# Optimization experiments

Measured on AMD Instinct MI355X. Metric: run time of the kernel, lower is better.

Reference implementation:

```python
import jax, jax.numpy as jnp
import numpy as np

B, S, E, H, T, VOCAB = 64, 512, 256, 512, 32, 32000

def setup_inputs():
    key = jax.random.key(0)
    ks = jax.random.split(key, 19)
    g = lambda i, shape: jax.random.normal(ks[i], shape, jnp.float32) * 0.05
    return {
        "sentence": jax.random.randint(ks[0], (S, B), 0, VOCAB),
        "emb_enc": g(1, (VOCAB, E)),
        "emb_dec": g(2, (VOCAB, E)),
        "W_ih": g(3, (4 * H, E)),
        "W_hh": g(4, (4 * H, H)),
        "b_ih": g(5, (4 * H,)),
        "b_hh": g(6, (4 * H,)),
        "dec_in0": g(7, (E,)),
        "Wx": g(8, (4 * H, E)),
        "bx": g(9, (4 * H,)),
        "Wh": g(10, (4 * H, H)),
        "bh": g(11, (4 * H,)),
        "W_out": g(12, (H, 2 * H)),
        "b_out": g(13, (H,)),
        "W_in": g(14, (H, H)),
        "b_in": g(15, (H,)),
        "W_ctx": g(16, (H, H)),
        "b_ctx": g(17, (H,)),
        "V": jax.random.uniform(ks[18], (H,), jnp.float32, -1.0, 1.0),
    }

def _lstm_cell(x, h, c, Wi, Whh, bi, bhh):
    # gate order i, f, g, o (matches torch LSTM and the decoder's chunk order)
    gates = x @ Wi.T + h @ Whh.T + bi + bhh
    i, f, g, o = jnp.split(gates, 4, axis=-1)
    c_t = jax.nn.sigmoid(f) * c + jax.nn.sigmoid(i) * jnp.tanh(g)
    h_t = jax.nn.sigmoid(o) * jnp.tanh(c_t)
    return h_t, c_t

def _pointer_net(sentence, emb_enc, emb_dec, W_ih, W_hh, b_ih, b_hh, dec_in0,
                 Wx, bx, Wh, bh, W_out, b_out, W_in, b_in, W_ctx, b_ctx, V):
    s_len, b = sentence.shape
    h_dim = W_hh.shape[1]
    embs = emb_enc[sentence]                          # [S, B, E]
    h0 = jnp.zeros((b, h_dim), embs.dtype)
    c0 = jnp.zeros((b, h_dim), embs.dtype)

    def enc_step(carry, x_t):
        h, c = _lstm_cell(x_t, carry[0], carry[1], W_ih, W_hh, b_ih, b_hh)
        return (h, c), h

    (h_n, c_n), enc_out = jax.lax.scan(enc_step, (h0, c0), embs)   # enc_out [S, B, H]
    context = enc_out.transpose(1, 0, 2)              # [B, S, H]
    # conv1d(kernel=1) projection of the context; constant across decode steps
    ctx = jnp.einsum('bsh,gh->bgs', context, W_ctx) + b_ctx[None, :, None]  # [B, H, S]

    dec_embs = emb_dec[sentence].transpose(1, 0, 2)   # [B, S, E]
    pos = jnp.arange(s_len)

    def dec_step(carry, _):
        dec_in, h, c, mask = carry
        h_t, c_t = _lstm_cell(dec_in, h, c, Wx, Wh, bx, bh)
        inp = h_t @ W_in.T + b_in                      # [B, H]
        att = jnp.einsum('h,bhs->bs', V, jnp.tanh(inp[:, :, None] + ctx))
        att = jnp.where(mask == 0, -jnp.inf, att)
        alpha = jax.nn.softmax(att, axis=1)            # [B, S]
        hidden_state = jnp.einsum('bhs,bs->bh', ctx, alpha)
        h_new = jnp.tanh(jnp.concatenate([hidden_state, h_t], axis=1) @ W_out.T + b_out)
        idx = jnp.argmax(alpha * mask, axis=1)         # greedy pointer, first max on ties
        one_hot = (pos[None, :] == idx[:, None]).astype(alpha.dtype)
        mask_new = mask * (1.0 - one_hot)
        next_in = jnp.take_along_axis(dec_embs, idx[:, None, None], axis=1)[:, 0, :]
        return (next_in, h_new, c_t, mask_new), (alpha, idx)

    mask0 = jnp.ones((b, s_len), embs.dtype)
    dec_in0_b = jnp.broadcast_to(dec_in0, (b, dec_in0.shape[0]))
    _, (alphas, ptrs) = jax.lax.scan(dec_step, (dec_in0_b, h_n, c_n, mask0), None, length=T)
    return alphas.transpose(1, 0, 2), ptrs.T          # [B, T, S], [B, T]

def reference(sentence, emb_enc, emb_dec, W_ih, W_hh, b_ih, b_hh, dec_in0,
              Wx, bx, Wh, bh, W_out, b_out, W_in, b_in, W_ctx, b_ctx, V):
    return _pointer_net(sentence, emb_enc, emb_dec, W_ih, W_hh, b_ih, b_hh, dec_in0,
                        Wx, bx, Wh, bh, W_out, b_out, W_in, b_in, W_ctx, b_ctx, V)
```

## Files before the change

### kernel.cpp

```cpp
#include <hip/hip_runtime.h>
#include <hip/hip_bf16.h>


typedef unsigned short u16;
typedef unsigned long long u64;
typedef __bf16 bf16_t;
typedef bf16_t bf16x8 __attribute__((ext_vector_type(8)));
typedef float f32x4 __attribute__((ext_vector_type(4)));

#define MFMA16(a, b, c) __builtin_amdgcn_mfma_f32_16x16x32_bf16(a, b, c, 0, 0, 0)
#define AGENT __HIP_MEMORY_SCOPE_AGENT

#define FLG_OFF   64u
#define GENE_OFF  128u
#define LDE_OFF   192u
#define FLE_OFF   1216u
#define GEND_OFF  11456u
#define LDD_OFF   11520u
#define FLD_OFF   12544u
#define BAR_END   28928u
#define HE_OFF    32768u
#define CW_OFF    294912u
#define HD_OFF    425984u
#define AO_OFF    557056u
#define INP_OFF   819200u
#define ATT_OFF   950272u
#define MSK_OFF   1081344u
#define PAC_OFF   1212416u
#define PML_OFF   1736704u
#define DIN_OFF   1740800u
#define CTX_OFF   2097152u
#define CTXL_OFF  (CTX_OFF + 33554432u)
#define NEED_T0   (CTX_OFF + 67108864u)
#define NEED_T1   (CTX_OFF + 50331648u)
#define NEED_T2   (CTX_OFF + 33554432u)

__device__ __forceinline__ float bf2f(u16 b) {
  union { unsigned u; float f; } c; c.u = ((unsigned)b) << 16; return c.f;
}
__device__ __forceinline__ u16 f2bf(float x) {
  union { float f; unsigned u; } c; c.f = x;
  unsigned r = c.u + 0x7FFFu + ((c.u >> 16) & 1u);
  return (u16)(r >> 16);
}
__device__ __forceinline__ float sigf(float x) { return 1.0f / (1.0f + expf(-x)); }
__device__ __forceinline__ float sel4(float a0, float a1, float a2, float a3, int j) {
  float r = (j == 1) ? a1 : a0;
  r = (j == 2) ? a2 : r;
  r = (j == 3) ? a3 : r;
  return r;
}
__device__ __forceinline__ float wget(const void* p, long i, int f32m) {
  return f32m ? ((const float*)p)[i] : bf2f(((const u16*)p)[i]);
}
__device__ __forceinline__ void ld8(const void* p, long i, int f32m, float (&o)[8]) {
  if (f32m) {
    const float4* q = (const float4*)((const float*)p + i);
    float4 a = q[0], b = q[1];
    o[0] = a.x; o[1] = a.y; o[2] = a.z; o[3] = a.w;
    o[4] = b.x; o[5] = b.y; o[6] = b.z; o[7] = b.w;
  } else {
    uint4 u = *(const uint4*)((const u16*)p + i);
    unsigned ww[4] = {u.x, u.y, u.z, u.w};
#pragma unroll
    for (int k = 0; k < 4; ++k) {
      o[2 * k] = bf2f((u16)(ww[k] & 0xFFFFu));
      o[2 * k + 1] = bf2f((u16)(ww[k] >> 16));
    }
  }
}
__device__ __forceinline__ float ald(const float* p) {
  return __hip_atomic_load(p, __ATOMIC_RELAXED, AGENT);
}
__device__ __forceinline__ void ast(float* p, float v) {
  __hip_atomic_store(p, v, __ATOMIC_RELAXED, AGENT);
}
__device__ __forceinline__ int aldi(const int* p) {
  return __hip_atomic_load(p, __ATOMIC_RELAXED, AGENT);
}
__device__ __forceinline__ void ld8T(const float* T, int kb, int bA, float (&o)[8]) {
  const float* p = T + kb * 64 + bA;
#pragma unroll
  for (int j = 0; j < 8; ++j) o[j] = ald(p + j * 64);
}

__device__ __forceinline__ void split3(float x, u16& h, u16& l, u16& l2) {
  union { float f; unsigned u; } c; c.f = x;
  h = (u16)(c.u >> 16);
  float r = x - bf2f(h);
  union { float f; unsigned u; } e; e.f = r;
  l = (u16)(e.u >> 16);
  float r2 = r - bf2f(l);
  union { float f; unsigned u; } g; g.f = r2;
  l2 = (u16)(g.u >> 16);
}
__device__ __forceinline__ void split8v(const float (&a)[8], bf16x8& H, bf16x8& L,
                                        bf16x8& L2) {
  union { unsigned u[4]; bf16x8 v; } hh, ll, mm;
#pragma unroll
  for (int k = 0; k < 4; ++k) {
    union { float f; unsigned u; } x0, x1;
    x0.f = a[2 * k]; x1.f = a[2 * k + 1];
    unsigned t0 = x0.u & 0xFFFF0000u, t1 = x1.u & 0xFFFF0000u;
    union { unsigned u; float f; } b0, b1; b0.u = t0; b1.u = t1;
    float r0 = x0.f - b0.f, r1 = x1.f - b1.f;
    union { float f; unsigned u; } e0, e1; e0.f = r0; e1.f = r1;
    unsigned s0 = e0.u & 0xFFFF0000u, s1 = e1.u & 0xFFFF0000u;
    union { unsigned u; float f; } c0, c1; c0.u = s0; c1.u = s1;
    float q0 = r0 - c0.f, q1 = r1 - c1.f;
    union { float f; unsigned u; } g0, g1; g0.f = q0; g1.f = q1;
    hh.u[k] = t1 | (x0.u >> 16);
    ll.u[k] = s1 | (e0.u >> 16);
    mm.u[k] = (g1.u & 0xFFFF0000u) | (g0.u >> 16);
  }
  H = hh.v; L = ll.v; L2 = mm.v;
}
// ... 4 lines not shown
  acc = MFMA16(al, bh, acc);
  acc = MFMA16(ah, bl, acc);
  acc = MFMA16(al, bl, acc);
  acc = MFMA16(ah, bl2, acc);
  acc = MFMA16(al2, bh, acc);
  return acc;
}
__device__ __forceinline__ f32x4 groupMMv(const float (&a8)[8], const u16* B3c, int bo,
                                          f32x4 acc) {
  bf16x8 H, L, L2;
  split8v(a8, H, L, L2);
  return mfma6(H, L, L2, *(const bf16x8*)(B3c + bo), *(const bf16x8*)(B3c + 4224 + bo),
               *(const bf16x8*)(B3c + 8448 + bo), acc);
}
__device__ __forceinline__ void stage16(u16* B3, const void* W, int f32m,
                                        long src, int n, int k16) {
  float t0[8], t1[8];
  ld8(W, src, f32m, t0);
  ld8(W, src + 8, f32m, t1);
#pragma unroll
  for (int j = 0; j < 8; ++j) {
    u16 h, l, l2; split3(t0[j], h, l, l2);
    int o = n * 264 + k16 + j;
    B3[o] = h; B3[4224 + o] = l; B3[8448 + o] = l2;
  }
#pragma unroll
  for (int j = 0; j < 8; ++j) {
    u16 h, l, l2; split3(t1[j], h, l, l2);
    int o = n * 264 + k16 + 8 + j;
    B3[o] = h; B3[4224 + o] = l; B3[8448 + o] = l2;
  }
}

__device__ __forceinline__ void ctx_store(char* ws, int tier, int oi, float x) {
  if (tier == 0) { ((float*)(ws + CTX_OFF))[oi] = x; return; }
  if (tier >= 3) return;
  u16 hi = f2bf(x);
  ((u16*)(ws + CTX_OFF))[oi] = hi;
  if (tier == 1) {
    unsigned e = hi & 0x7F80u; if (e == 0) e = 0x0080u;
    float us = bf2f((u16)e) * 0.00390625f;
    float r = (x - bf2f(hi)) / us;
    int q = (int)__float2int_rn(r * 254.0f);
    q = max(-127, min(127, q));
    ((signed char*)(ws + CTXL_OFF))[oi] = (signed char)q;
  }
}
__device__ __forceinline__ void ctx_load8(const char* ws, int tier, int oi, float (&cx)[8]) {
  if (tier == 0) {
    const float4* p = (const float4*)((const float*)(ws + CTX_OFF) + oi);
    float4 a = p[0], b = p[1];
    cx[0] = a.x; cx[1] = a.y; cx[2] = a.z; cx[3] = a.w;
    cx[4] = b.x; cx[5] = b.y; cx[6] = b.z; cx[7] = b.w;
    return;
  }
  if (tier >= 3) {
#pragma unroll
    for (int j = 0; j < 8; ++j) cx[j] = 0.0f;
    return;
  }
  uint4 hu = *(const uint4*)((const u16*)(ws + CTX_OFF) + oi);
  unsigned hw[4] = {hu.x, hu.y, hu.z, hu.w};
  u16 h[8];
#pragma unroll
  for (int k = 0; k < 4; ++k) { h[2*k] = (u16)(hw[k] & 0xFFFFu); h[2*k+1] = (u16)(hw[k] >> 16); }
#pragma unroll
  for (int j = 0; j < 8; ++j) cx[j] = bf2f(h[j]);
  if (tier == 1) {
    const signed char* lp = (const signed char*)(ws + CTXL_OFF) + oi;
#pragma unroll
    for (int j = 0; j < 8; ++j) {
      unsigned e = h[j] & 0x7F80u; if (e == 0) e = 0x0080u;
      float us = bf2f((u16)e) * 0.00390625f;
      cx[j] += (float)lp[j] * us * (1.0f / 254.0f);
    }
  }
}

__device__ __forceinline__ void fbar_arrive(char* ws, unsigned flOff, int wg, int gen) {
  __builtin_amdgcn_s_waitcnt(0);
  __syncthreads();
  if (threadIdx.x == 0)
    __hip_atomic_store((int*)(ws + flOff) + wg * 16, gen, __ATOMIC_RELAXED, AGENT);
}
__device__ __forceinline__ void fbar_wait(char* ws, unsigned flOff, int nwg, int gen) {
  const int tid = threadIdx.x;
  if (tid < 64) {
    const int* fl = (const int*)(ws + flOff);
    for (int i = tid; i < nwg; i += 64) {
      const int* f = fl + i * 16;
      while (aldi(f) < gen) __builtin_amdgcn_s_sleep(1);
    }
  }
  __syncthreads();
}

__global__ void prep_detect(const void* embE, char* ws) {
  __shared__ int cnt;
  if (threadIdx.x == 0) cnt = 0;
  __syncthreads();
  const u16* p = (const u16*)embE;
  int c = 0;
  for (int i = threadIdx.x; i < 4096; i += 256) {
    float v = bf2f(p[i]);
    if (!(fabsf(v) < 4.0f)) c++;
  }
  atomicAdd(&cnt, c);
  __syncthreads();
  if (threadIdx.x == 0) *(int*)(ws + FLG_OFF) = (cnt > 200) ? 1 : 0;
}

__global__ void prep_init(const void* din0, char* ws) {
  const int f32m = *(const int*)(ws + FLG_OFF);
  int i0 = blockIdx.x * 256 + threadIdx.x;
  int stride = gridDim.x * 256;
  int* bars = (int*)ws;
  for (int i = i0; i < (int)((BAR_END - GENE_OFF) / 4); i += stride)
    bars[(GENE_OFF / 4) + i] = 0;
  float* h0 = (float*)(ws + HE_OFF);
  float* mask = (float*)(ws + MSK_OFF);
  float* dinT = (float*)(ws + DIN_OFF);
  for (int i = i0; i < 32768; i += stride) { h0[i] = 0.0f; mask[i] = 1.0f; }
  for (int i = i0; i < 16384; i += stride) dinT[i] = wget(din0, i >> 6, f32m);
}

__global__ __launch_bounds__(256, 1) void enc_pers(
    const int* __restrict__ sent, const void* __restrict__ embE,
    const void* __restrict__ Wih, const void* __restrict__ Whh,
    const void* __restrict__ bih, const void* __restrict__ bhh,
    const void* __restrict__ Wctx, const void* __restrict__ bctx,
    char* __restrict__ ws, int tier) {
  __shared__ __align__(16) u16 B3[38016];
  const int tid = threadIdx.x, w = blockIdx.x;
  const int f32m = *(const int*)(ws + FLG_OFF);
  const int lane = tid & 63, v = tid >> 6, ln15 = lane & 15, q = lane >> 4;
  const int bA = v * 16 + ln15;
  const int sn = tid >> 4, sk = (tid & 15) * 16;
  float* heT = (float*)(ws + HE_OFF);
  float* cwp = (float*)(ws + CW_OFF);

  const int g = ln15 & 3;
  const int unit = w * 4 + (ln15 >> 2);
  float creg[4];
#pragma unroll
  for (int r = 0; r < 4; ++r) creg[r] = 0.0f;
  float bias = 0.0f;

  if (w < 128) {
    long grC = (long)(g * 512 + unit);
    bias = wget(bih, grC, f32m) + wget(bhh, grC, f32m);
    const long grS = (long)((sn & 3) * 512 + w * 4 + (sn >> 2));
    stage16(B3, Wih, f32m, grS * 256 + sk, sn, sk);
    stage16(B3 + 12672, Whh, f32m, grS * 512 + sk, sn, sk);
    stage16(B3 + 25344, Whh, f32m, grS * 512 + 256 + sk, sn, sk);
  } else {
    const long grS = (long)((w - 128) * 16 + sn);
    stage16(B3, Wctx, f32m, grS * 512 + sk, sn, sk);
    stage16(B3 + 12672, Wctx, f32m, grS * 512 + 256 + sk, sn, sk);
  }
  __syncthreads();

#pragma unroll 1
  for (int t = 0; t < 512; ++t) {
    const int slot = t & 1;
    const float* hsT = heT + slot * 32768;
    if (w < 128) {
      const int tok = sent[t * 64 + bA];
      f32x4 acc = {0.f, 0.f, 0.f, 0.f};
      {
        float aE[4][8];
#pragma unroll
        for (int pf = 0; pf < 3; ++pf)
          ld8(embE, (long)tok * 256 + pf * 32 + q * 8, f32m, aE[pf]);
#pragma unroll
        for (int ks = 0; ks < 8; ++ks) {
          if (ks + 3 < 8) ld8(embE, (long)tok * 256 + (ks + 3) * 32 + q * 8, f32m,
                              aE[(ks + 3) & 3]);
          acc = groupMMv(aE[ks & 3], B3, ln15 * 264 + ks * 32 + q * 8, acc);
        }
      }
      if (t) fbar_wait(ws, FLE_OFF, 160, t);
      {
        float aH[4][8];
#pragma unroll
        for (int pf = 0; pf < 3; ++pf) ld8T(hsT, pf * 32 + q * 8, bA, aH[pf]);
#pragma unroll
        for (int kk = 0; kk < 16; ++kk) {
          if (kk + 3 < 16) ld8T(hsT, (kk + 3) * 32 + q * 8, bA, aH[(kk + 3) & 3]);
          acc = groupMMv(aH[kk & 3], B3 + (1 + (kk >> 3)) * 12672,
                         ln15 * 264 + (kk & 7) * 32 + q * 8, acc);
        }
      }
      float* hdTs = heT + (slot ^ 1) * 32768;
#pragma unroll
      for (int r = 0; r < 4; ++r) {
        int br = v * 16 + q * 4 + r;
        float val = acc[r] + bias;
        float x1 = __shfl_xor(val, 1);
        float x2 = __shfl_xor(val, 2);
        float x3 = __shfl_xor(val, 3);
        float gi = sel4(val, x1, x2, x3, g);
        float gf = sel4(val, x1, x2, x3, g ^ 1);
        float gg = sel4(val, x1, x2, x3, g ^ 2);
        float go = sel4(val, x1, x2, x3, g ^ 3);
        float cn = sigf(gf) * creg[r] + sigf(gi) * tanhf(gg);
        float hv = sigf(go) * tanhf(cn);
        creg[r] = cn;
        if (g == 0) ast(hdTs + unit * 64 + br, hv);
      }
    } else {
      if (t) {
        fbar_wait(ws, FLE_OFF, 160, t);
        float aH[4][8];
#pragma unroll
        for (int pf = 0; pf < 3; ++pf) ld8T(hsT, pf * 32 + q * 8, bA, aH[pf]);
        f32x4 acc = {0.f, 0.f, 0.f, 0.f};
#pragma unroll
        for (int kk = 0; kk < 16; ++kk) {
          if (kk + 3 < 16) ld8T(hsT, (kk + 3) * 32 + q * 8, bA, aH[(kk + 3) & 3]);
          acc = groupMMv(aH[kk & 3], B3 + (kk >> 3) * 12672,
                         ln15 * 264 + (kk & 7) * 32 + q * 8, acc);
        }
        const int d = (w - 128) * 16 + ln15;
        float bb = wget(bctx, d, f32m);
#pragma unroll
        for (int r = 0; r < 4; ++r) {
          int br = v * 16 + q * 4 + r;
          ctx_store(ws, tier, (br * 512 + (t - 1)) * 512 + d, acc[r] + bb);
        }
      }
    }
    fbar_arrive(ws, FLE_OFF, w, t + 1);
  }
  if (w >= 128) {
    fbar_wait(ws, FLE_OFF, 160, 512);
    const float* hsT = heT;
    float aH[4][8];
#pragma unroll
    for (int pf = 0; pf < 3; ++pf) ld8T(hsT, pf * 32 + q * 8, bA, aH[pf]);
    f32x4 acc = {0.f, 0.f, 0.f, 0.f};
#pragma unroll
    for (int kk = 0; kk < 16; ++kk) {
      if (kk + 3 < 16) ld8T(hsT, (kk + 3) * 32 + q * 8, bA, aH[(kk + 3) & 3]);
      acc = groupMMv(aH[kk & 3], B3 + (kk >> 3) * 12672,
                     ln15 * 264 + (kk & 7) * 32 + q * 8, acc);
    }
    const int d = (w - 128) * 16 + ln15;
    float bb = wget(bctx, d, f32m);
#pragma unroll
    for (int r = 0; r < 4; ++r) {
      int br = v * 16 + q * 4 + r;
      ctx_store(ws, tier, (br * 512 + 511) * 512 + d, acc[r] + bb);
    }
  } else if (g == 0) {
#pragma unroll
    for (int r = 0; r < 4; ++r) cwp[(v * 16 + q * 4 + r) * 512 + unit] = creg[r];
  }
}

__global__ __launch_bounds__(256, 1) void dec_pers(
    const int* __restrict__ sent, const void* __restrict__ embD,
    const void* __restrict__ Wx, const void* __restrict__ bx,
    const void* __restrict__ Wh, const void* __restrict__ bh,
    const void* __restrict__ Wout, const void* __restrict__ bout,
    const void* __restrict__ Win, const void* __restrict__ bin,
    const void* __restrict__ V, char* __restrict__ ws,
    float* __restrict__ out, int tier) {
  __shared__ __align__(16) u16 B3[50688];
  __shared__ float accL[512];
  __shared__ float mlL[8];
  __shared__ float redA[256];
  __shared__ int redI[256];

  const int tid = threadIdx.x, wg = blockIdx.x;
  const int f32m = *(const int*)(ws + FLG_OFF);
  const int lane = tid & 63, v = tid >> 6, ln15 = lane & 15, q = lane >> 4;
  const int bA = v * 16 + ln15;
  const int sn = tid >> 4, sk = (tid & 15) * 16;
  float* hdT = (float*)(ws + HD_OFF);
  float* aoT = (float*)(ws + AO_OFF);
  float* inp = (float*)(ws + INP_OFF);
  float* att = (float*)(ws + ATT_OFF);
  float* mask = (float*)(ws + MSK_OFF);
  float* pac = (float*)(ws + PAC_OFF);
  float* pml = (float*)(ws + PML_OFF);
  float* dinT = (float*)(ws + DIN_OFF);
  const float* hnT = (const float*)(ws + HE_OFF);
  int bgen = 0;

  const int g = ln15 & 3;
  const int unit = (wg < 128) ? (wg * 4 + (ln15 >> 2)) : 0;
  float creg[4];
  float bias = 0.0f;
  if (wg < 128) {
    const float* cwp = (const float*)(ws + CW_OFF);
#pragma unroll
    for (int r = 0; r < 4; ++r) creg[r] = cwp[(v * 16 + q * 4 + r) * 512 + unit];
    bias = wget(bx, (long)(g * 512 + unit), f32m) + wget(bh, (long)(g * 512 + unit), f32m);
  }
  float vj[8];
#pragma unroll
  for (int j = 0; j < 8; ++j) vj[j] = wget(V, lane * 8 + j, f32m);

  if (wg < 128) {
    const long grS = (long)((sn & 3) * 512 + wg * 4 + (sn >> 2));
    stage16(B3, Wx, f32m, grS * 256 + sk, sn, sk);
    stage16(B3 + 12672, Wh, f32m, grS * 512 + sk, sn, sk);
    stage16(B3 + 25344, Wh, f32m, grS * 512 + 256 + sk, sn, sk);
  } else if (wg < 160) {
    const long grS = (long)((wg - 128) * 16 + sn);
    stage16(B3, Win, f32m, grS * 512 + sk, sn, sk);
    stage16(B3 + 12672, Win, f32m, grS * 512 + 256 + sk, sn, sk);
  } else if (wg < 192) {
    const long grS = (long)((wg - 160) * 16 + sn);
#pragma unroll
    for (int cc = 0; cc < 4; ++cc)
      stage16(B3 + cc * 12672, Wout, f32m, grS * 1024 + cc * 256 + sk, sn, sk);
  }
  __syncthreads();

  f32x4 acc1 = {0.f, 0.f, 0.f, 0.f};
  if (wg < 128) {
    float aD[4][8];
#pragma unroll
    for (int pf = 0; pf < 3; ++pf) ld8T(dinT, pf * 32 + q * 8, bA, aD[pf]);
#pragma unroll
    for (int ks = 0; ks < 8; ++ks) {
      if (ks + 3 < 8) ld8T(dinT, (ks + 3) * 32 + q * 8, bA, aD[(ks + 3) & 3]);
      acc1 = groupMMv(aD[ks & 3], B3, ln15 * 264 + ks * 32 + q * 8, acc1);
    }
  }

#pragma unroll 1
  for (int t = 0; t < 32; ++t) {
    if (wg < 128) {
      const float* hsT = (t == 0) ? hnT : (const float*)hdT;
      float aH[4][8];
#pragma unroll
      for (int pf = 0; pf < 3; ++pf) ld8T(hsT, pf * 32 + q * 8, bA, aH[pf]);
#pragma unroll
      for (int kk = 0; kk < 16; ++kk) {
        if (kk + 3 < 16) ld8T(hsT, (kk + 3) * 32 + q * 8, bA, aH[(kk + 3) & 3]);
        acc1 = groupMMv(aH[kk & 3], B3 + (1 + (kk >> 3)) * 12672,
                        ln15 * 264 + (kk & 7) * 32 + q * 8, acc1);
      }
#pragma unroll
      for (int r = 0; r < 4; ++r) {
        int br = v * 16 + q * 4 + r;
        float val = acc1[r] + bias;
        float x1 = __shfl_xor(val, 1);
        float x2 = __shfl_xor(val, 2);
        float x3 = __shfl_xor(val, 3);
        float gi = sel4(val, x1, x2, x3, g);
        float gf = sel4(val, x1, x2, x3, g ^ 1);
        float gg = sel4(val, x1, x2, x3, g ^ 2);
        float go = sel4(val, x1, x2, x3, g ^ 3);
        float cn = sigf(gf) * creg[r] + sigf(gi) * tanhf(gg);
        float hv = sigf(go) * tanhf(cn);
        creg[r] = cn;
        if (g == 0) ast(aoT + (512 + unit) * 64 + br, hv);
      }
    }
    ++bgen;
    fbar_arrive(ws, FLD_OFF, wg, bgen);
    fbar_wait(ws, FLD_OFF, 256, bgen);
    if (wg >= 128 && wg < 160) {
      float aH[4][8];
#pragma unroll
      for (int pf = 0; pf < 3; ++pf) ld8T(aoT, 512 + pf * 32 + q * 8, bA, aH[pf]);
      f32x4 acc = {0.f, 0.f, 0.f, 0.f};
#pragma unroll
      for (int kk = 0; kk < 16; ++kk) {
        if (kk + 3 < 16) ld8T(aoT, 512 + (kk + 3) * 32 + q * 8, bA, aH[(kk + 3) & 3]);
        acc = groupMMv(aH[kk & 3], B3 + (kk >> 3) * 12672,
                       ln15 * 264 + (kk & 7) * 32 + q * 8, acc);
      }
      const int d = (wg - 128) * 16 + ln15;
      float bb = wget(bin, d, f32m);
#pragma unroll
      for (int r = 0; r < 4; ++r)
        ast(inp + (v * 16 + q * 4 + r) * 512 + d, acc[r] + bb);
    }
    ++bgen;
    fbar_arrive(ws, FLD_OFF, wg, bgen);
    const int b = wg & 63, qq = wg >> 6;
    const int s0 = qq * 128 + v * 32;
    float mkB[4];
    float cxB[4][8];
#pragma unroll
    for (int pf = 0; pf < 3; ++pf) {
      mkB[pf] = ald(mask + b * 512 + s0 + pf);
      ctx_load8(ws, tier, (b * 512 + s0 + pf) * 512 + lane * 8, cxB[pf]);
    }
    fbar_wait(ws, FLD_OFF, 256, bgen);
    {
      float ij[8];
#pragma unroll
      for (int j = 0; j < 8; ++j) ij[j] = ald(inp + b * 512 + lane * 8 + j);
      for (int i = tid; i < 512; i += 256) accL[i] = 0.0f;
      __syncthreads();
      float m = -1e30f, l = 0.0f;
      float oacc[8];
#pragma unroll
      for (int j = 0; j < 8; ++j) oacc[j] = 0.0f;
#pragma unroll 1
      for (int i0 = 0; i0 < 32; ++i0) {
        const int s = s0 + i0;
        if (i0 + 3 < 32) {
          mkB[(i0 + 3) & 3] = ald(mask + b * 512 + s + 3);
          ctx_load8(ws, tier, (b * 512 + s + 3) * 512 + lane * 8, cxB[(i0 + 3) & 3]);
        }
        float mkC = mkB[i0 & 3];
        const float (&cxC)[8] = cxB[i0 & 3];
        if (mkC == 0.0f) {
          if (lane == 0) ast(att + b * 512 + s, -1e30f);
        } else {
          float p = 0.0f;
#pragma unroll
          for (int j = 0; j < 8; ++j) p += vj[j] * tanhf(ij[j] + cxC[j]);
#pragma unroll
          for (int off = 1; off < 64; off <<= 1) p += __shfl_xor(p, off);
          if (lane == 0) ast(att + b * 512 + s, p);
          if (p <= m) {
            float e = expf(p - m);
            l += e;
#pragma unroll
            for (int j = 0; j < 8; ++j) oacc[j] += e * cxC[j];
          } else {
            float sc = expf(m - p);
            l = l * sc + 1.0f;
#pragma unroll
            for (int j = 0; j < 8; ++j) oacc[j] = oacc[j] * sc + cxC[j];
            m = p;
          }
        }
      }
      if (lane == 0) { mlL[v * 2] = m; mlL[v * 2 + 1] = l; }
      __syncthreads();
      float M = fmaxf(fmaxf(mlL[0], mlL[2]), fmaxf(mlL[4], mlL[6]));
      float Lq = 0.0f;
#pragma unroll
      for (int vv = 0; vv < 4; ++vv) Lq += mlL[vv * 2 + 1] * expf(mlL[vv * 2] - M);
      float scv = expf(m - M);
      for (int vv = 0; vv < 4; ++vv) {
        if (v == vv) {
#pragma unroll
          for (int j = 0; j < 8; ++j) accL[lane * 8 + j] += oacc[j] * scv;
        }
        __syncthreads();
      }
      for (int i = tid; i < 512; i += 256) ast(pac + (b * 4 + qq) * 512 + i, accL[i]);
      if (tid == 0) {
        ast(pml + (b * 4 + qq) * 2, M);
        ast(pml + (b * 4 + qq) * 2 + 1, Lq);
      }
    }
    ++bgen;
    fbar_arrive(ws, FLD_OFF, wg, bgen);
    fbar_wait(ws, FLD_OFF, 256, bgen);
    if (wg < 64) {
      const int bb = wg;
      float m0 = ald(pml + (bb * 4 + 0) * 2), m1 = ald(pml + (bb * 4 + 1) * 2);
      float m2 = ald(pml + (bb * 4 + 2) * 2), m3 = ald(pml + (bb * 4 + 3) * 2);
      float l0 = ald(pml + (bb * 4 + 0) * 2 + 1), l1 = ald(pml + (bb * 4 + 1) * 2 + 1);
      float l2 = ald(pml + (bb * 4 + 2) * 2 + 1), l3 = ald(pml + (bb * 4 + 3) * 2 + 1);
      float M = fmaxf(fmaxf(m0, m1), fmaxf(m2, m3));
      float e0 = expf(m0 - M), e1 = expf(m1 - M), e2 = expf(m2 - M), e3 = expf(m3 - M);
      float L = l0 * e0 + l1 * e1 + l2 * e2 + l3 * e3;
      L = fmaxf(L, 1e-30f);
      for (int h = tid; h < 512; h += 256) {
        float hv = (ald(pac + (bb * 4 + 0) * 512 + h) * e0 +
                    ald(pac + (bb * 4 + 1) * 512 + h) * e1 +
                    ald(pac + (bb * 4 + 2) * 512 + h) * e2 +
                    ald(pac + (bb * 4 + 3) * 512 + h) * e3) / L;
        ast(aoT + h * 64 + bb, hv);
      }
      float bestA = -1.0f;
      int bestS = 0;
#pragma unroll
      for (int k = 0; k < 2; ++k) {
        int s = tid * 2 + k;
        float a = expf(ald(att + bb * 512 + s) - M) / L;
        out[(bb * 32 + t) * 512 + s] = a;
        if (a > bestA) { bestA = a; bestS = s; }
      }
      redA[tid] = bestA;
      redI[tid] = bestS;
      __syncthreads();
      for (int st = 128; st > 0; st >>= 1) {
        if (tid < st) {
          if (redA[tid + st] > redA[tid]) { redA[tid] = redA[tid + st]; redI[tid] = redI[tid + st]; }
        }
        __syncthreads();
      }
      int idx = redI[0];
      if (tid == 0) {
        ast(mask + bb * 512 + idx, 0.0f);
        out[1048576 + bb * 32 + t] = (float)idx;
      }
      int token = sent[idx * 64 + bb];
      ast(dinT + tid * 64 + bb, wget(embD, (long)token * 256 + tid, f32m));
    }
    ++bgen;
    fbar_arrive(ws, FLD_OFF, wg, bgen);
    fbar_wait(ws, FLD_OFF, 256, bgen);
    if (wg >= 160 && wg < 192) {
      float aH[4][8];
#pragma unroll
      for (int pf = 0; pf < 3; ++pf) ld8T(aoT, pf * 32 + q * 8, bA, aH[pf]);
      f32x4 acc = {0.f, 0.f, 0.f, 0.f};
#pragma unroll
      for (int kk = 0; kk < 32; ++kk) {
        if (kk + 3 < 32) ld8T(aoT, (kk + 3) * 32 + q * 8, bA, aH[(kk + 3) & 3]);
        acc = groupMMv(aH[kk & 3], B3 + (kk >> 3) * 12672,
                       ln15 * 264 + (kk & 7) * 32 + q * 8, acc);
      }
      const int d = (wg - 160) * 16 + ln15;
      float bb = wget(bout, d, f32m);
#pragma unroll
      for (int r = 0; r < 4; ++r)
        ast(hdT + d * 64 + (v * 16 + q * 4 + r), tanhf(acc[r] + bb));
    }
    ++bgen;
    fbar_arrive(ws, FLD_OFF, wg, bgen);
    if (wg < 128 && t < 31) {
      float aD[4][8];
#pragma unroll
      for (int pf = 0; pf < 3; ++pf) ld8T(dinT, pf * 32 + q * 8, bA, aD[pf]);
      f32x4 accn = {0.f, 0.f, 0.f, 0.f};
#pragma unroll
      for (int ks = 0; ks < 8; ++ks) {
        if (ks + 3 < 8) ld8T(dinT, (ks + 3) * 32 + q * 8, bA, aD[(ks + 3) & 3]);
        accn = groupMMv(aD[ks & 3], B3, ln15 * 264 + ks * 32 + q * 8, accn);
      }
      acc1 = accn;
    }
    if (t < 31) fbar_wait(ws, FLD_OFF, 256, bgen);
  }
}

__global__ void diag_kernel(char* ws, float* out, int wsMiB) {
  if (threadIdx.x == 0 && blockIdx.x == 0) {
    int f = *(int*)(ws + FLG_OFF);
    out[0] = (float)(wsMiB + 2000 * f);
  }
}

extern "C" void kernel_launch(void* const* d_in, const int* in_sizes, int n_in,
                              void* d_out, int out_size, void* d_ws, size_t ws_size,
                              hipStream_t stream) {
  (void)in_sizes; (void)n_in; (void)out_size;
  const int* sent = (const int*)d_in[0];
  const void* embE = d_in[1];
  const void* embD = d_in[2];
  const void* Wih = d_in[3];
  const void* Whh = d_in[4];
  const void* bih = d_in[5];
  const void* bhh = d_in[6];
  const void* din0 = d_in[7];
  const void* Wx = d_in[8];
  const void* bx = d_in[9];
  const void* Wh = d_in[10];
  const void* bh = d_in[11];
  const void* Wout = d_in[12];
  const void* bout = d_in[13];
  const void* Win = d_in[14];
  const void* bin = d_in[15];
  const void* Wctx = d_in[16];
  const void* bctx = d_in[17];
  const void* V = d_in[18];
// ... 19 lines not shown
```

Baseline: 8.893 ms.

## Decouple encoder context projection, stage hidden states in LDS, use hierarchical barrier

The encoder gate workgroups now wait only on each other plus a lagged context flag, and the W_ctx projection workgroups run behind them through a triple-buffered hidden state. Before, all 160 workgroups shared one lockstep barrier every step. Matrix operands that were read with strided per-element atomic loads are now read with coalesced 64-bit loads, staged through padded shared memory, and prefetched one chunk ahead. The decoder's flat barrier, where every workgroup polled all 256 flags, becomes a two-level tree. In exchange the kernels use more LDS and add extra __syncthreads inside each GEMM, and the three-slot buffer depends on the lag flags being correct.

```diff
diff --git a/kernel.cpp b/kernel.cpp
--- a/kernel.cpp
+++ b/kernel.cpp
@@ -12,23 +12,22 @@
 #define AGENT __HIP_MEMORY_SCOPE_AGENT
 
 #define FLG_OFF   64u
-#define GENE_OFF  128u
-#define LDE_OFF   192u
-#define FLE_OFF   1216u
-#define GEND_OFF  11456u
-#define LDD_OFF   11520u
-#define FLD_OFF   12544u
-#define BAR_END   28928u
+#define FLE_OFF   128u
+#define FLC_OFF   8320u
+#define LDD_OFF   10368u
+#define GEND_OFF  11392u
+#define FLD_OFF   11520u
+#define BAR_END   27904u
 #define HE_OFF    32768u
-#define CW_OFF    294912u
-#define HD_OFF    425984u
-#define AO_OFF    557056u
-#define INP_OFF   819200u
-#define ATT_OFF   950272u
-#define MSK_OFF   1081344u
-#define PAC_OFF   1212416u
-#define PML_OFF   1736704u
-#define DIN_OFF   1740800u
+#define CW_OFF    425984u
+#define HD_OFF    557056u
+#define AO_OFF    688128u
+#define INP_OFF   950272u
+#define ATT_OFF   1081344u
+#define MSK_OFF   1212416u
+#define PAC_OFF   1343488u
+#define PML_OFF   1867776u
+#define DIN_OFF   1871872u
 #define CTX_OFF   2097152u
 #define CTXL_OFF  (CTX_OFF + 33554432u)
 #define NEED_T0   (CTX_OFF + 67108864u)
@@ -77,11 +76,6 @@
 }
 __device__ __forceinline__ int aldi(const int* p) {
   return __hip_atomic_load(p, __ATOMIC_RELAXED, AGENT);
-}
-__device__ __forceinline__ void ld8T(const float* T, int kb, int bA, float (&o)[8]) {
-  const float* p = T + kb * 64 + bA;
-#pragma unroll
-  for (int j = 0; j < 8; ++j) o[j] = ald(p + j * 64);
 }
 
 __device__ __forceinline__ void split3(float x, u16& h, u16& l, u16& l2) {
@@ -152,6 +146,53 @@
   }
 }
 
+__device__ __forceinline__ f32x4 gemmStaged(const float* __restrict__ T,
+    const u16* __restrict__ B3, int kgoff, int ng, float* __restrict__ hS,
+    int tid, int ln15, int q, int bA, f32x4 acc) {
+  const int nch = ng >> 2;
+  u64 pend[16];
+#pragma unroll
+  for (int i = 0; i < 16; ++i)
+    pend[i] = __hip_atomic_load((const u64*)T + i * 256 + tid,
+                                __ATOMIC_RELAXED, AGENT);
+  __syncthreads();
+#pragma unroll
+  for (int i = 0; i < 16; ++i) {
+    int gi = i * 256 + tid;
+    ((u64*)hS)[(gi >> 5) * 33 + (gi & 31)] = pend[i];
+  }
+  __syncthreads();
+#pragma unroll 1
+  for (int c = 0; c < nch; ++c) {
+    if (c + 1 < nch) {
+#pragma unroll
+      for (int i = 0; i < 16; ++i)
+        pend[i] = __hip_atomic_load((const u64*)T + (c + 1) * 4096 + i * 256 + tid,
+                                    __ATOMIC_RELAXED, AGENT);
+    }
+#pragma unroll
+    for (int k4 = 0; k4 < 4; ++k4) {
+      const int kg = c * 4 + k4 + kgoff;
+      float a8[8];
+#pragma unroll
+      for (int j = 0; j < 8; ++j)
+        a8[j] = hS[(k4 * 32 + q * 8 + j) * 66 + bA];
+      acc = groupMMv(a8, B3 + (kg >> 3) * 12672,
+                     ln15 * 264 + (kg & 7) * 32 + q * 8, acc);
+    }
+    if (c + 1 < nch) {
+      __syncthreads();
+#pragma unroll
+      for (int i = 0; i < 16; ++i) {
+        int gi = i * 256 + tid;
+        ((u64*)hS)[(gi >> 5) * 33 + (gi & 31)] = pend[i];
+      }
+      __syncthreads();
+    }
+  }
+  return acc;
+}
+
 __device__ __forceinline__ void ctx_store(char* ws, int tier, int oi, float x) {
   if (tier == 0) { ((float*)(ws + CTX_OFF))[oi] = x; return; }
   if (tier >= 3) return;
@@ -197,20 +238,60 @@
   }
 }
 
-__device__ __forceinline__ void fbar_arrive(char* ws, unsigned flOff, int wg, int gen) {
+__device__ __forceinline__ void enc_arrive(char* ws, unsigned off, int idx, int gen) {
   __builtin_amdgcn_s_waitcnt(0);
   __syncthreads();
   if (threadIdx.x == 0)
-    __hip_atomic_store((int*)(ws + flOff) + wg * 16, gen, __ATOMIC_RELAXED, AGENT);
-}
-__device__ __forceinline__ void fbar_wait(char* ws, unsigned flOff, int nwg, int gen) {
+    __hip_atomic_store((int*)(ws + off) + idx * 16, gen, __ATOMIC_RELAXED, AGENT);
+}
+__device__ __forceinline__ void gate_wait(char* ws, int gen, int genc) {
+  const int tid = threadIdx.x;
+  if (tid < 128) {
+    const int* f = (const int*)(ws + FLE_OFF) + tid * 16;
+    while (aldi(f) < gen) __builtin_amdgcn_s_sleep(2);
+  } else if (tid < 160 && genc > 0) {
+    const int* f = (const int*)(ws + FLC_OFF) + (tid - 128) * 16;
+    while (aldi(f) < genc) __builtin_amdgcn_s_sleep(2);
+  }
+  __syncthreads();
+}
+__device__ __forceinline__ void ctx_wait(char* ws, int gen) {
+  const int tid = threadIdx.x;
+  if (tid < 128) {
+    const int* f = (const int*)(ws + FLE_OFF) + tid * 16;
+    while (aldi(f) < gen) __builtin_amdgcn_s_sleep(2);
+  }
+  __syncthreads();
+}
+
+__device__ __forceinline__ void sbar_arrive(char* ws, int wg, int gen) {
+  __builtin_amdgcn_s_waitcnt(0);
+  __syncthreads();
+  if (threadIdx.x == 0)
+    __hip_atomic_store((int*)(ws + FLD_OFF) + wg * 16, gen, __ATOMIC_RELAXED, AGENT);
+}
+__device__ __forceinline__ void sbar_wait(char* ws, int wg, int gen) {
   const int tid = threadIdx.x;
   if (tid < 64) {
-    const int* fl = (const int*)(ws + flOff);
-    for (int i = tid; i < nwg; i += 64) {
-      const int* f = fl + i * 16;
-      while (aldi(f) < gen) __builtin_amdgcn_s_sleep(1);
-    }
+    int* fl = (int*)(ws + FLD_OFF);
+    int* ldv = (int*)(ws + LDD_OFF);
+    int* gp = (int*)(ws + GEND_OFF);
+    if (wg < 16) {
+      if (tid < 16) {
+        const int* f = &fl[(wg + (tid << 4)) * 16];
+        while (aldi(f) < gen) __builtin_amdgcn_s_sleep(2);
+      }
+      if (tid == 0) __hip_atomic_store(&ldv[wg * 16], gen, __ATOMIC_RELAXED, AGENT);
+    }
+    if (wg == 0) {
+      if (tid < 16) {
+        const int* f = &ldv[tid * 16];
+        while (aldi(f) < gen) __builtin_amdgcn_s_sleep(2);
+      }
+      if (tid == 0) __hip_atomic_store(gp, gen, __ATOMIC_RELAXED, AGENT);
+    }
+    if (tid == 0)
+      while (aldi((const int*)gp) < gen) __builtin_amdgcn_s_sleep(2);
   }
   __syncthreads();
 }
@@ -235,12 +316,13 @@
   int i0 = blockIdx.x * 256 + threadIdx.x;
   int stride = gridDim.x * 256;
   int* bars = (int*)ws;
-  for (int i = i0; i < (int)((BAR_END - GENE_OFF) / 4); i += stride)
-    bars[(GENE_OFF / 4) + i] = 0;
-  float* h0 = (float*)(ws + HE_OFF);
+  for (int i = i0; i < (int)((BAR_END - FLE_OFF) / 4); i += stride)
+    bars[(FLE_OFF / 4) + i] = 0;
+  float* he = (float*)(ws + HE_OFF);
   float* mask = (float*)(ws + MSK_OFF);
   float* dinT = (float*)(ws + DIN_OFF);
-  for (int i = i0; i < 32768; i += stride) { h0[i] = 0.0f; mask[i] = 1.0f; }
+  for (int i = i0; i < 98304; i += stride) he[i] = 0.0f;
+  for (int i = i0; i < 32768; i += stride) mask[i] = 1.0f;
   for (int i = i0; i < 16384; i += stride) dinT[i] = wget(din0, i >> 6, f32m);
 }
 
@@ -251,6 +333,7 @@
     const void* __restrict__ Wctx, const void* __restrict__ bctx,
     char* __restrict__ ws, int tier) {
   __shared__ __align__(16) u16 B3[38016];
+  __shared__ __align__(16) float hS[8448];
   const int tid = threadIdx.x, w = blockIdx.x;
   const int f32m = *(const int*)(ws + FLG_OFF);
   const int lane = tid & 63, v = tid >> 6, ln15 = lane & 15, q = lane >> 4;
@@ -261,31 +344,23 @@
 
   const int g = ln15 & 3;
   const int unit = w * 4 + (ln15 >> 2);
-  float creg[4];
-#pragma unroll
-  for (int r = 0; r < 4; ++r) creg[r] = 0.0f;
-  float bias = 0.0f;
 
   if (w < 128) {
+    float creg[4];
+#pragma unroll
+    for (int r = 0; r < 4; ++r) creg[r] = 0.0f;
     long grC = (long)(g * 512 + unit);
-    bias = wget(bih, grC, f32m) + wget(bhh, grC, f32m);
+    float bias = wget(bih, grC, f32m) + wget(bhh, grC, f32m);
     const long grS = (long)((sn & 3) * 512 + w * 4 + (sn >> 2));
     stage16(B3, Wih, f32m, grS * 256 + sk, sn, sk);
     stage16(B3 + 12672, Whh, f32m, grS * 512 + sk, sn, sk);
     stage16(B3 + 25344, Whh, f32m, grS * 512 + 256 + sk, sn, sk);
-  } else {
-    const long grS = (long)((w - 128) * 16 + sn);
-    stage16(B3, Wctx, f32m, grS * 512 + sk, sn, sk);
-    stage16(B3 + 12672, Wctx, f32m, grS * 512 + 256 + sk, sn, sk);
-  }
-  __syncthreads();
-
+    __syncthreads();
+
+    int sR = 2, sW = 0;
 #pragma unroll 1
-  for (int t = 0; t < 512; ++t) {
-    const int slot = t & 1;
-    const float* hsT = heT + slot * 32768;
-    if (w < 128) {
-      const int tok = sent[t * 64 + bA];
+    for (int u = 0; u < 512; ++u) {
+      const int tok = sent[u * 64 + bA];
       f32x4 acc = {0.f, 0.f, 0.f, 0.f};
       {
         float aE[4][8];
@@ -299,19 +374,9 @@
           acc = groupMMv(aE[ks & 3], B3, ln15 * 264 + ks * 32 + q * 8, acc);
         }
       }
-      if (t) fbar_wait(ws, FLE_OFF, 160, t);
-      {
-        float aH[4][8];
-#pragma unroll
-        for (int pf = 0; pf < 3; ++pf) ld8T(hsT, pf * 32 + q * 8, bA, aH[pf]);
-#pragma unroll
-        for (int kk = 0; kk < 16; ++kk) {
-          if (kk + 3 < 16) ld8T(hsT, (kk + 3) * 32 + q * 8, bA, aH[(kk + 3) & 3]);
-          acc = groupMMv(aH[kk & 3], B3 + (1 + (kk >> 3)) * 12672,
-                         ln15 * 264 + (kk & 7) * 32 + q * 8, acc);
-        }
-      }
-      float* hdTs = heT + (slot ^ 1) * 32768;
+      if (u) gate_wait(ws, u, u - 1);
+      acc = gemmStaged(heT + sR * 32768, B3, 8, 16, hS, tid, ln15, q, bA, acc);
+      float* hdTs = heT + sW * 32768;
 #pragma unroll
       for (int r = 0; r < 4; ++r) {
         int br = v * 16 + q * 4 + r;
@@ -328,53 +393,35 @@
         creg[r] = cn;
         if (g == 0) ast(hdTs + unit * 64 + br, hv);
       }
-    } else {
-      if (t) {
-        fbar_wait(ws, FLE_OFF, 160, t);
-        float aH[4][8];
-#pragma unroll
-        for (int pf = 0; pf < 3; ++pf) ld8T(hsT, pf * 32 + q * 8, bA, aH[pf]);
-        f32x4 acc = {0.f, 0.f, 0.f, 0.f};
-#pragma unroll
-        for (int kk = 0; kk < 16; ++kk) {
-          if (kk + 3 < 16) ld8T(hsT, (kk + 3) * 32 + q * 8, bA, aH[(kk + 3) & 3]);
-          acc = groupMMv(aH[kk & 3], B3 + (kk >> 3) * 12672,
-                         ln15 * 264 + (kk & 7) * 32 + q * 8, acc);
-        }
-        const int d = (w - 128) * 16 + ln15;
-        float bb = wget(bctx, d, f32m);
-#pragma unroll
-        for (int r = 0; r < 4; ++r) {
-          int br = v * 16 + q * 4 + r;
-          ctx_store(ws, tier, (br * 512 + (t - 1)) * 512 + d, acc[r] + bb);
-        }
-      }
-    }
-    fbar_arrive(ws, FLE_OFF, w, t + 1);
-  }
-  if (w >= 128) {
-    fbar_wait(ws, FLE_OFF, 160, 512);
-    const float* hsT = heT;
-    float aH[4][8];
-#pragma unroll
-    for (int pf = 0; pf < 3; ++pf) ld8T(hsT, pf * 32 + q * 8, bA, aH[pf]);
-    f32x4 acc = {0.f, 0.f, 0.f, 0.f};
-#pragma unroll
-    for (int kk = 0; kk < 16; ++kk) {
-      if (kk + 3 < 16) ld8T(hsT, (kk + 3) * 32 + q * 8, bA, aH[(kk + 3) & 3]);
-      acc = groupMMv(aH[kk & 3], B3 + (kk >> 3) * 12672,
-                     ln15 * 264 + (kk & 7) * 32 + q * 8, acc);
-    }
-    const int d = (w - 128) * 16 + ln15;
+      enc_arrive(ws, FLE_OFF, w, u + 1);
+      sR = sW; sW = (sW == 2) ? 0 : sW + 1;
+    }
+    if (g == 0) {
+#pragma unroll
+      for (int r = 0; r < 4; ++r) cwp[(v * 16 + q * 4 + r) * 512 + unit] = creg[r];
+    }
+  } else {
+    const int w2 = w - 128;
+    const long grS = (long)(w2 * 16 + sn);
+    stage16(B3, Wctx, f32m, grS * 512 + sk, sn, sk);
+    stage16(B3 + 12672, Wctx, f32m, grS * 512 + 256 + sk, sn, sk);
+    __syncthreads();
+    const int d = w2 * 16 + ln15;
     float bb = wget(bctx, d, f32m);
-#pragma unroll
-    for (int r = 0; r < 4; ++r) {
-      int br = v * 16 + q * 4 + r;
-      ctx_store(ws, tier, (br * 512 + 511) * 512 + d, acc[r] + bb);
-    }
-  } else if (g == 0) {
-#pragma unroll
-    for (int r = 0; r < 4; ++r) cwp[(v * 16 + q * 4 + r) * 512 + unit] = creg[r];
+    int sC = 0;
+#pragma unroll 1
+    for (int vv = 0; vv < 512; ++vv) {
+      ctx_wait(ws, vv + 1);
+      f32x4 acc = {0.f, 0.f, 0.f, 0.f};
+      acc = gemmStaged(heT + sC * 32768, B3, 0, 16, hS, tid, ln15, q, bA, acc);
+#pragma unroll
+      for (int r = 0; r < 4; ++r) {
+        int br = v * 16 + q * 4 + r;
+        ctx_store(ws, tier, (br * 512 + vv) * 512 + d, acc[r] + bb);
+      }
+      enc_arrive(ws, FLC_OFF, w2, vv + 1);
+      sC = (sC == 2) ? 0 : sC + 1;
+    }
   }
 }
 
@@ -387,6 +434,7 @@
     const void* __restrict__ V, char* __restrict__ ws,
     float* __restrict__ out, int tier) {
   __shared__ __align__(16) u16 B3[50688];
+  __shared__ __align__(16) float hS[8448];
   __shared__ float accL[512];
   __shared__ float mlL[8];
   __shared__ float redA[256];
@@ -405,7 +453,7 @@
   float* pac = (float*)(ws + PAC_OFF);
   float* pml = (float*)(ws + PML_OFF);
   float* dinT = (float*)(ws + DIN_OFF);
-  const float* hnT = (const float*)(ws + HE_OFF);
+  const float* hnT = (const float*)(ws + HE_OFF) + 32768;
   int bgen = 0;
 
   const int g = ln15 & 3;
@@ -440,30 +488,14 @@
   __syncthreads();
 
   f32x4 acc1 = {0.f, 0.f, 0.f, 0.f};
-  if (wg < 128) {
-    float aD[4][8];
-#pragma unroll
-    for (int pf = 0; pf < 3; ++pf) ld8T(dinT, pf * 32 + q * 8, bA, aD[pf]);
-#pragma unroll
-    for (int ks = 0; ks < 8; ++ks) {
-      if (ks + 3 < 8) ld8T(dinT, (ks + 3) * 32 + q * 8, bA, aD[(ks + 3) & 3]);
-      acc1 = groupMMv(aD[ks & 3], B3, ln15 * 264 + ks * 32 + q * 8, acc1);
-    }
-  }
+  if (wg < 128)
+    acc1 = gemmStaged(dinT, B3, 0, 8, hS, tid, ln15, q, bA, acc1);
 
 #pragma unroll 1
   for (int t = 0; t < 32; ++t) {
     if (wg < 128) {
       const float* hsT = (t == 0) ? hnT : (const float*)hdT;
-      float aH[4][8];
-#pragma unroll
-      for (int pf = 0; pf < 3; ++pf) ld8T(hsT, pf * 32 + q * 8, bA, aH[pf]);
-#pragma unroll
-      for (int kk = 0; kk < 16; ++kk) {
-        if (kk + 3 < 16) ld8T(hsT, (kk + 3) * 32 + q * 8, bA, aH[(kk + 3) & 3]);
-        acc1 = groupMMv(aH[kk & 3], B3 + (1 + (kk >> 3)) * 12672,
-                        ln15 * 264 + (kk & 7) * 32 + q * 8, acc1);
-      }
+      acc1 = gemmStaged(hsT, B3, 8, 16, hS, tid, ln15, q, bA, acc1);
 #pragma unroll
       for (int r = 0; r < 4; ++r) {
         int br = v * 16 + q * 4 + r;
@@ -482,19 +514,11 @@
       }
     }
     ++bgen;
-    fbar_arrive(ws, FLD_OFF, wg, bgen);
-    fbar_wait(ws, FLD_OFF, 256, bgen);
+    sbar_arrive(ws, wg, bgen);
+    sbar_wait(ws, wg, bgen);
     if (wg >= 128 && wg < 160) {
-      float aH[4][8];
-#pragma unroll
-      for (int pf = 0; pf < 3; ++pf) ld8T(aoT, 512 + pf * 32 + q * 8, bA, aH[pf]);
       f32x4 acc = {0.f, 0.f, 0.f, 0.f};
-#pragma unroll
-      for (int kk = 0; kk < 16; ++kk) {
-        if (kk + 3 < 16) ld8T(aoT, 512 + (kk + 3) * 32 + q * 8, bA, aH[(kk + 3) & 3]);
-        acc = groupMMv(aH[kk & 3], B3 + (kk >> 3) * 12672,
-                       ln15 * 264 + (kk & 7) * 32 + q * 8, acc);
-      }
+      acc = gemmStaged((const float*)aoT + 32768, B3, 0, 16, hS, tid, ln15, q, bA, acc);
       const int d = (wg - 128) * 16 + ln15;
       float bb = wget(bin, d, f32m);
 #pragma unroll
@@ -502,7 +526,7 @@
         ast(inp + (v * 16 + q * 4 + r) * 512 + d, acc[r] + bb);
     }
     ++bgen;
-    fbar_arrive(ws, FLD_OFF, wg, bgen);
+    sbar_arrive(ws, wg, bgen);
     const int b = wg & 63, qq = wg >> 6;
     const int s0 = qq * 128 + v * 32;
     float mkB[4];
@@ -512,7 +536,7 @@
       mkB[pf] = ald(mask + b * 512 + s0 + pf);
       ctx_load8(ws, tier, (b * 512 + s0 + pf) * 512 + lane * 8, cxB[pf]);
     }
-    fbar_wait(ws, FLD_OFF, 256, bgen);
+    sbar_wait(ws, wg, bgen);
     {
       float ij[8];
 #pragma unroll
@@ -576,8 +600,8 @@
       }
     }
     ++bgen;
-    fbar_arrive(ws, FLD_OFF, wg, bgen);
-    fbar_wait(ws, FLD_OFF, 256, bgen);
+    sbar_arrive(ws, wg, bgen);
+    sbar_wait(ws, wg, bgen);
     if (wg < 64) {
       const int bb = wg;
       float m0 = ald(pml + (bb * 4 + 0) * 2), m1 = ald(pml + (bb * 4 + 1) * 2);
@@ -622,40 +646,25 @@
       ast(dinT + tid * 64 + bb, wget(embD, (long)token * 256 + tid, f32m));
     }
     ++bgen;
-    fbar_arrive(ws, FLD_OFF, wg, bgen);
-    fbar_wait(ws, FLD_OFF, 256, bgen);
+    sbar_arrive(ws, wg, bgen);
+    sbar_wait(ws, wg, bgen);
     if (wg >= 160 && wg < 192) {
-      float aH[4][8];
-#pragma unroll
-      for (int pf = 0; pf < 3; ++pf) ld8T(aoT, pf * 32 + q * 8, bA, aH[pf]);
       f32x4 acc = {0.f, 0.f, 0.f, 0.f};
-#pragma unroll
-      for (int kk = 0; kk < 32; ++kk) {
-        if (kk + 3 < 32) ld8T(aoT, (kk + 3) * 32 + q * 8, bA, aH[(kk + 3) & 3]);
-        acc = groupMMv(aH[kk & 3], B3 + (kk >> 3) * 12672,
-                       ln15 * 264 + (kk & 7) * 32 + q * 8, acc);
-      }
+      acc = gemmStaged((const float*)aoT, B3, 0, 32, hS, tid, ln15, q, bA, acc);
       const int d = (wg - 160) * 16 + ln15;
-      float bb = wget(bout, d, f32m);
+      float bb2 = wget(bout, d, f32m);
 #pragma unroll
       for (int r = 0; r < 4; ++r)
-        ast(hdT + d * 64 + (v * 16 + q * 4 + r), tanhf(acc[r] + bb));
+        ast(hdT + d * 64 + (v * 16 + q * 4 + r), tanhf(acc[r] + bb2));
     }
     ++bgen;
-    fbar_arrive(ws, FLD_OFF, wg, bgen);
+    sbar_arrive(ws, wg, bgen);
     if (wg < 128 && t < 31) {
-      float aD[4][8];
-#pragma unroll
-      for (int pf = 0; pf < 3; ++pf) ld8T(dinT, pf * 32 + q * 8, bA, aD[pf]);
       f32x4 accn = {0.f, 0.f, 0.f, 0.f};
-#pragma unroll
-      for (int ks = 0; ks < 8; ++ks) {
-        if (ks + 3 < 8) ld8T(dinT, (ks + 3) * 32 + q * 8, bA, aD[(ks + 3) & 3]);
-        accn = groupMMv(aD[ks & 3], B3, ln15 * 264 + ks * 32 + q * 8, accn);
-      }
+      accn = gemmStaged(dinT, B3, 0, 8, hS, tid, ln15, q, bA, accn);
       acc1 = accn;
     }
-    if (t < 31) fbar_wait(ws, FLD_OFF, 256, bgen);
+    if (t < 31) sbar_wait(ws, wg, bgen);
   }
 }
 
```

Result: slower. 9.206 ms (+3.5%).

## Use hierarchical decoder barrier with acquire fences and plain loads; split softmax combine

Applied to the files above, without the earlier changes.

Replaces the flat 256-workgroup flag barrier in the decoder loop with a two-level barrier: 16 leader workgroups each gather 16 flags, then everyone polls 16 leader flags. Relaxed atomic loads of shared buffers become plain loads (vectorised for inp), with an agent-scope acquire fence after each barrier for visibility. The attention-context combine is moved from the 64 argmax workgroups to 64 other workgroups so it runs alongside the argmax and embedding fetch. This cuts polling traffic and serial work per step, at the cost of an extra barrier level and reliance on the fences for correctness.

```diff
diff --git a/kernel.cpp b/kernel.cpp
--- a/kernel.cpp
+++ b/kernel.cpp
@@ -13,9 +13,7 @@
 
 #define FLG_OFF   64u
 #define GENE_OFF  128u
-#define LDE_OFF   192u
 #define FLE_OFF   1216u
-#define GEND_OFF  11456u
 #define LDD_OFF   11520u
 #define FLD_OFF   12544u
 #define BAR_END   28928u
@@ -69,19 +67,22 @@
     }
   }
 }
-__device__ __forceinline__ float ald(const float* p) {
-  return __hip_atomic_load(p, __ATOMIC_RELAXED, AGENT);
-}
 __device__ __forceinline__ void ast(float* p, float v) {
   __hip_atomic_store(p, v, __ATOMIC_RELAXED, AGENT);
 }
 __device__ __forceinline__ int aldi(const int* p) {
   return __hip_atomic_load(p, __ATOMIC_RELAXED, AGENT);
 }
+__device__ __forceinline__ void asti(int* p, int v) {
+  __hip_atomic_store(p, v, __ATOMIC_RELAXED, AGENT);
+}
+__device__ __forceinline__ void acq_fence() {
+  __builtin_amdgcn_fence(__ATOMIC_ACQUIRE, "agent");
+}
 __device__ __forceinline__ void ld8T(const float* T, int kb, int bA, float (&o)[8]) {
   const float* p = T + kb * 64 + bA;
 #pragma unroll
-  for (int j = 0; j < 8; ++j) o[j] = ald(p + j * 64);
+  for (int j = 0; j < 8; ++j) o[j] = p[j * 64];
 }
 
 __device__ __forceinline__ void split3(float x, u16& h, u16& l, u16& l2) {
@@ -201,7 +202,7 @@
   __builtin_amdgcn_s_waitcnt(0);
   __syncthreads();
   if (threadIdx.x == 0)
-    __hip_atomic_store((int*)(ws + flOff) + wg * 16, gen, __ATOMIC_RELAXED, AGENT);
+    asti((int*)(ws + flOff) + wg * 16, gen);
 }
 __device__ __forceinline__ void fbar_wait(char* ws, unsigned flOff, int nwg, int gen) {
   const int tid = threadIdx.x;
@@ -212,6 +213,32 @@
       while (aldi(f) < gen) __builtin_amdgcn_s_sleep(1);
     }
   }
+  __syncthreads();
+  acq_fence();
+  __syncthreads();
+}
+
+__device__ __forceinline__ void dbar_arrive(char* ws, int wg, int gen) {
+  __builtin_amdgcn_s_waitcnt(0);
+  __syncthreads();
+  if (threadIdx.x == 0)
+    asti((int*)(ws + FLD_OFF) + wg * 16, gen);
+}
+__device__ __forceinline__ void dbar_wait(char* ws, int wg, int gen) {
+  const int tid = threadIdx.x;
+  if (wg < 16) {
+    if (tid < 16) {
+      const int* f = (const int*)(ws + FLD_OFF) + (wg * 16 + tid) * 16;
+      while (aldi(f) < gen) __builtin_amdgcn_s_sleep(1);
+    }
+    if (tid == 0) asti((int*)(ws + LDD_OFF) + wg * 16, gen);
+  }
+  if (tid < 16) {
+    const int* f = (const int*)(ws + LDD_OFF) + tid * 16;
+    while (aldi(f) < gen) __builtin_amdgcn_s_sleep(2);
+  }
+  __syncthreads();
+  acq_fence();
   __syncthreads();
 }
 
@@ -482,8 +509,8 @@
       }
     }
     ++bgen;
-    fbar_arrive(ws, FLD_OFF, wg, bgen);
-    fbar_wait(ws, FLD_OFF, 256, bgen);
+    dbar_arrive(ws, wg, bgen);
+    dbar_wait(ws, wg, bgen);
     if (wg >= 128 && wg < 160) {
       float aH[4][8];
 #pragma unroll
@@ -502,21 +529,25 @@
         ast(inp + (v * 16 + q * 4 + r) * 512 + d, acc[r] + bb);
     }
     ++bgen;
-    fbar_arrive(ws, FLD_OFF, wg, bgen);
+    dbar_arrive(ws, wg, bgen);
     const int b = wg & 63, qq = wg >> 6;
     const int s0 = qq * 128 + v * 32;
     float mkB[4];
     float cxB[4][8];
 #pragma unroll
     for (int pf = 0; pf < 3; ++pf) {
-      mkB[pf] = ald(mask + b * 512 + s0 + pf);
+      mkB[pf] = mask[b * 512 + s0 + pf];
       ctx_load8(ws, tier, (b * 512 + s0 + pf) * 512 + lane * 8, cxB[pf]);
     }
-    fbar_wait(ws, FLD_OFF, 256, bgen);
+    dbar_wait(ws, wg, bgen);
     {
       float ij[8];
-#pragma unroll
-      for (int j = 0; j < 8; ++j) ij[j] = ald(inp + b * 512 + lane * 8 + j);
+      {
+        const float4* qp = (const float4*)(inp + b * 512 + lane * 8);
+        float4 a = qp[0], c = qp[1];
+        ij[0] = a.x; ij[1] = a.y; ij[2] = a.z; ij[3] = a.w;
+        ij[4] = c.x; ij[5] = c.y; ij[6] = c.z; ij[7] = c.w;
+      }
       for (int i = tid; i < 512; i += 256) accL[i] = 0.0f;
       __syncthreads();
       float m = -1e30f, l = 0.0f;
@@ -527,7 +558,7 @@
       for (int i0 = 0; i0 < 32; ++i0) {
         const int s = s0 + i0;
         if (i0 + 3 < 32) {
-          mkB[(i0 + 3) & 3] = ald(mask + b * 512 + s + 3);
+          mkB[(i0 + 3) & 3] = mask[b * 512 + s + 3];
           ctx_load8(ws, tier, (b * 512 + s + 3) * 512 + lane * 8, cxB[(i0 + 3) & 3]);
         }
         float mkC = mkB[i0 & 3];
@@ -576,31 +607,45 @@
       }
     }
     ++bgen;
-    fbar_arrive(ws, FLD_OFF, wg, bgen);
-    fbar_wait(ws, FLD_OFF, 256, bgen);
-    if (wg < 64) {
-      const int bb = wg;
-      float m0 = ald(pml + (bb * 4 + 0) * 2), m1 = ald(pml + (bb * 4 + 1) * 2);
-      float m2 = ald(pml + (bb * 4 + 2) * 2), m3 = ald(pml + (bb * 4 + 3) * 2);
-      float l0 = ald(pml + (bb * 4 + 0) * 2 + 1), l1 = ald(pml + (bb * 4 + 1) * 2 + 1);
-      float l2 = ald(pml + (bb * 4 + 2) * 2 + 1), l3 = ald(pml + (bb * 4 + 3) * 2 + 1);
+    dbar_arrive(ws, wg, bgen);
+    dbar_wait(ws, wg, bgen);
+    if (wg >= 64 && wg < 128) {
+      const int j = wg - 64;
+      const int bb = tid & 63;
+      float m0 = pml[(bb * 4 + 0) * 2], m1 = pml[(bb * 4 + 1) * 2];
+      float m2 = pml[(bb * 4 + 2) * 2], m3 = pml[(bb * 4 + 3) * 2];
+      float l0 = pml[(bb * 4 + 0) * 2 + 1], l1 = pml[(bb * 4 + 1) * 2 + 1];
+      float l2 = pml[(bb * 4 + 2) * 2 + 1], l3 = pml[(bb * 4 + 3) * 2 + 1];
       float M = fmaxf(fmaxf(m0, m1), fmaxf(m2, m3));
       float e0 = expf(m0 - M), e1 = expf(m1 - M), e2 = expf(m2 - M), e3 = expf(m3 - M);
       float L = l0 * e0 + l1 * e1 + l2 * e2 + l3 * e3;
       L = fmaxf(L, 1e-30f);
-      for (int h = tid; h < 512; h += 256) {
-        float hv = (ald(pac + (bb * 4 + 0) * 512 + h) * e0 +
-                    ald(pac + (bb * 4 + 1) * 512 + h) * e1 +
-                    ald(pac + (bb * 4 + 2) * 512 + h) * e2 +
-                    ald(pac + (bb * 4 + 3) * 512 + h) * e3) / L;
+#pragma unroll
+      for (int k = 0; k < 2; ++k) {
+        int h = j * 8 + (tid >> 6) * 2 + k;
+        float hv = (pac[(bb * 4 + 0) * 512 + h] * e0 +
+                    pac[(bb * 4 + 1) * 512 + h] * e1 +
+                    pac[(bb * 4 + 2) * 512 + h] * e2 +
+                    pac[(bb * 4 + 3) * 512 + h] * e3) / L;
         ast(aoT + h * 64 + bb, hv);
       }
+    }
+    if (wg < 64) {
+      const int bb = wg;
+      float m0 = pml[(bb * 4 + 0) * 2], m1 = pml[(bb * 4 + 1) * 2];
+      float m2 = pml[(bb * 4 + 2) * 2], m3 = pml[(bb * 4 + 3) * 2];
+      float l0 = pml[(bb * 4 + 0) * 2 + 1], l1 = pml[(bb * 4 + 1) * 2 + 1];
+      float l2 = pml[(bb * 4 + 2) * 2 + 1], l3 = pml[(bb * 4 + 3) * 2 + 1];
+      float M = fmaxf(fmaxf(m0, m1), fmaxf(m2, m3));
+      float e0 = expf(m0 - M), e1 = expf(m1 - M), e2 = expf(m2 - M), e3 = expf(m3 - M);
+      float L = l0 * e0 + l1 * e1 + l2 * e2 + l3 * e3;
+      L = fmaxf(L, 1e-30f);
       float bestA = -1.0f;
       int bestS = 0;
 #pragma unroll
       for (int k = 0; k < 2; ++k) {
         int s = tid * 2 + k;
-        float a = expf(ald(att + bb * 512 + s) - M) / L;
+        float a = expf(att[bb * 512 + s] - M) / L;
         out[(bb * 32 + t) * 512 + s] = a;
         if (a > bestA) { bestA = a; bestS = s; }
       }
@@ -622,8 +667,8 @@
       ast(dinT + tid * 64 + bb, wget(embD, (long)token * 256 + tid, f32m));
     }
     ++bgen;
-    fbar_arrive(ws, FLD_OFF, wg, bgen);
-    fbar_wait(ws, FLD_OFF, 256, bgen);
+    dbar_arrive(ws, wg, bgen);
+    dbar_wait(ws, wg, bgen);
     if (wg >= 160 && wg < 192) {
       float aH[4][8];
 #pragma unroll
@@ -636,13 +681,13 @@
                        ln15 * 264 + (kk & 7) * 32 + q * 8, acc);
       }
       const int d = (wg - 160) * 16 + ln15;
-      float bb = wget(bout, d, f32m);
+      float bb2 = wget(bout, d, f32m);
 #pragma unroll
       for (int r = 0; r < 4; ++r)
-        ast(hdT + d * 64 + (v * 16 + q * 4 + r), tanhf(acc[r] + bb));
+        ast(hdT + d * 64 + (v * 16 + q * 4 + r), tanhf(acc[r] + bb2));
     }
     ++bgen;
-    fbar_arrive(ws, FLD_OFF, wg, bgen);
+    dbar_arrive(ws, wg, bgen);
     if (wg < 128 && t < 31) {
       float aD[4][8];
 #pragma unroll
@@ -655,7 +700,7 @@
       }
       acc1 = accn;
     }
-    if (t < 31) fbar_wait(ws, FLD_OFF, 256, bgen);
+    if (t < 31) dbar_wait(ws, wg, bgen);
   }
 }
 
```

Measured after the change: 11.72 ms. 31.8% more time.
